# Kernel optimization log

Measured on AMD Instinct MI355X. Metric: run time of the kernel, lower is better.

## Reference

```python
import jax, jax.numpy as jnp
import numpy as np

B = 16384
IN = 1024      # feature_count * embedding_dim
E = 6          # expert_numb
D = 20         # domain_numb
EH1, EH2 = 256, 128
EO = 10        # expert_out_dim
GH = 64        # gate hidden
TH = 64        # tower hidden
TO = 1         # tower_output_dim


def setup_inputs() -> dict:
    key = jax.random.key(0)
    ks = jax.random.split(key, 20)
    s = lambda k, shp, fan: jax.random.normal(k, shp, jnp.float32) * (1.0 / np.sqrt(fan))
    return {
        "x": jax.random.normal(ks[0], (B, IN), jnp.float32),
        "domain_id": jax.random.randint(ks[1], (B,), 0, D, jnp.int64 if jax.config.jax_enable_x64 else jnp.int32),
        # expert MLPs: IN -> 256 -> 128 -> EO, ReLU hidden, no final act
        "Ew1": s(ks[2], (E, IN, EH1), IN), "Eb1": jnp.zeros((E, EH1), jnp.float32),
        "Ew2": s(ks[3], (E, EH1, EH2), EH1), "Eb2": jnp.zeros((E, EH2), jnp.float32),
        "Ew3": s(ks[4], (E, EH2, EO), EH2), "Eb3": jnp.zeros((E, EO), jnp.float32),
        # gate MLPs: IN -> 64 -> E, ReLU hidden, softmax applied in forward
        "Gw1": s(ks[5], (D, IN, GH), IN), "Gb1": jnp.zeros((D, GH), jnp.float32),
        "Gw2": s(ks[6], (D, GH, E), GH), "Gb2": jnp.zeros((D, E), jnp.float32),
        # tower MLPs: EO -> 64 -> 1, ReLU hidden, Sigmoid final
        "Tw1": s(ks[7], (D, EO, TH), EO), "Tb1": jnp.zeros((D, TH), jnp.float32),
        "Tw2": s(ks[8], (D, TH, TO), TH), "Tb2": jnp.zeros((D, TO), jnp.float32),
    }


def _forward(x, Ew1, Eb1, Ew2, Eb2, Ew3, Eb3, Gw1, Gb1, Gw2, Gb2, Tw1, Tb1, Tw2, Tb2, domain_id):
    # Experts: all E experts on every sample. eo: [E, B, EO]
    h = jax.nn.relu(jnp.einsum('bi,eih->ebh', x, Ew1) + Eb1[:, None, :])
    h = jax.nn.relu(jnp.einsum('ebh,ehk->ebk', h, Ew2) + Eb2[:, None, :])
    eo = jnp.einsum('ebk,eko->ebo', h, Ew3) + Eb3[:, None, :]
    # Gates: all D domain gates, softmax over expert axis. gate: [D, B, E]
    g = jax.nn.relu(jnp.einsum('bi,dih->dbh', x, Gw1) + Gb1[:, None, :])
    gate = jax.nn.softmax(jnp.einsum('dbh,dhe->dbe', g, Gw2) + Gb2[:, None, :], axis=-1)
    # MMoE combine per domain: [D, B, EO]
    mmoe = jnp.einsum('dbe,ebo->dbo', gate, eo)
    # Towers: all D towers. tout: [D, B, TO]
    th = jax.nn.relu(jnp.einsum('dbo,doh->dbh', mmoe, Tw1) + Tb1[:, None, :])
    tout = jax.nn.sigmoid(jnp.einsum('dbh,dho->dbo', th, Tw2) + Tb2[:, None, :])
    # Gather per-sample domain (discard 19/20 of tower & mmoe outputs)
    b_idx = jnp.arange(x.shape[0])
    selected_outputs = tout[domain_id, b_idx]   # [B, TO]
    selected_mmoe = mmoe[domain_id, b_idx]      # [B, EO]
    avg_expert_repr = jnp.mean(eo, axis=0)      # [B, EO]
    return selected_outputs, avg_expert_repr, selected_mmoe


def reference(x, domain_id, Ew1, Eb1, Ew2, Eb2, Ew3, Eb3, Gw1, Gb1, Gw2, Gb2, Tw1, Tb1, Tw2, Tb2):
    return _forward(x, Ew1, Eb1, Ew2, Eb2, Ew3, Eb3, Gw1, Gb1, Gw2, Gb2, Tw1, Tb1, Tw2, Tb2, domain_id)
```

## Files before the change

### kernel.cpp

```cpp
#include <hip/hip_runtime.h>
#include <hip/hip_bf16.h>
#include <math.h>

#define B_    16384
#define IN_   1024
#define E_    6
#define D_    20
#define EH1_  256
#define EH2_  128
#define EO_   10
#define GH_   64
#define TH_   64

typedef short  s16x8  __attribute__((ext_vector_type(8)));
typedef float  f32x4  __attribute__((ext_vector_type(4)));
typedef float  f32x16 __attribute__((ext_vector_type(16)));

__device__ inline ushort f2bf(float f) {
    union { float f; uint32_t u; } v; v.f = f;
    return (ushort)((v.u + 0x7fffu + ((v.u >> 16) & 1u)) >> 16);
}

#define GLOBAL_LDS16(g, l)                                                     \
    __builtin_amdgcn_global_load_lds(                                          \
        (const __attribute__((address_space(1))) void*)(g),                    \
        (__attribute__((address_space(3))) void*)(l), 16, 0, 0)

#define NCHUNK (B_ / 256)

#define CVT_BLKS  2048
#define CVT_ITERS (B_ * IN_ / 4 / 256 / CVT_BLKS)
#define WT1_TILES ((EH1_ / 32) * (IN_ / 32) * E_)
#define WT2_TILES ((EH2_ / 32) * (EH1_ / 32) * E_)
#define WTG_TILES ((GH_ / 32) * (IN_ / 32) * D_)
#define PREP_BLKS (CVT_BLKS + WT1_TILES + WT2_TILES + WTG_TILES + NCHUNK)

__global__ __launch_bounds__(256) void k_prep(
        const float* __restrict__ x, ushort* __restrict__ xb,
        const float* __restrict__ Ew1, ushort* __restrict__ W1t,
        const float* __restrict__ Ew2, ushort* __restrict__ W2t,
        const float* __restrict__ Gw1, ushort* __restrict__ G1t,
        const int* __restrict__ dom, int* __restrict__ cnts) {
    __shared__ float tile[32][33];
    __shared__ int hcnt[D_];
    int bid = blockIdx.x;
    const int t = threadIdx.x;

    if (bid < CVT_BLKS) {
        int i = bid * 256 + t;
        #pragma unroll
        for (int it = 0; it < CVT_ITERS; ++it, i += CVT_BLKS * 256) {
            float4 v = ((const float4*)x)[i];
            ushort4 o;
            o.x = f2bf(v.x); o.y = f2bf(v.y); o.z = f2bf(v.z); o.w = f2bf(v.w);
            ((ushort4*)xb)[i] = o;
        }
        return;
    }
    bid -= CVT_BLKS;

    const float* W; ushort* Wt; int K, N, z, ky, nx;
    if (bid < WT1_TILES) {
        W = Ew1; Wt = W1t; K = IN_; N = EH1_;
        z = bid / (8 * 32); int r = bid % (8 * 32); ky = r / 8; nx = r % 8;
    } else if (bid < WT1_TILES + WT2_TILES) {
        bid -= WT1_TILES;
        W = Ew2; Wt = W2t; K = EH1_; N = EH2_;
        z = bid / (4 * 8); int r = bid % (4 * 8); ky = r / 4; nx = r % 4;
    } else if (bid < WT1_TILES + WT2_TILES + WTG_TILES) {
        bid -= WT1_TILES + WT2_TILES;
        W = Gw1; Wt = G1t; K = IN_; N = GH_;
        z = bid / (2 * 32); int r = bid % (2 * 32); ky = r / 2; nx = r % 2;
    } else {
        int c = bid - (WT1_TILES + WT2_TILES + WTG_TILES);
        if (t < D_) hcnt[t] = 0;
        __syncthreads();
        atomicAdd(&hcnt[dom[c * 256 + t]], 1);
        __syncthreads();
        if (t < D_) cnts[c * D_ + t] = hcnt[t];
        return;
    }
    const int n0 = nx * 32, k0 = ky * 32;
    const float* We = W + (size_t)z * K * N;
    ushort* Wte = Wt + (size_t)z * K * N;
    const int lx = t & 31, ly = t >> 5;
    #pragma unroll
    for (int r = 0; r < 4; ++r)
        tile[ly + r * 8][lx] = We[(size_t)(k0 + ly + r * 8) * N + n0 + lx];
    __syncthreads();
    #pragma unroll
    for (int r = 0; r < 4; ++r)
        Wte[(size_t)(n0 + ly + r * 8) * K + k0 + lx] = f2bf(tile[lx][ly + r * 8]);
}

#define GBK 32
#define H2P 136

__global__ __launch_bounds__(256) void k_gemm(
        const ushort* __restrict__ A, const ushort* __restrict__ Wt,
        const float* __restrict__ Bias, ushort* __restrict__ C,
        const int* __restrict__ dom, const int* __restrict__ cnts,
        int* __restrict__ perm, int* __restrict__ gbaseG,
        int* __restrict__ histG, int* __restrict__ gtab,
        int* __restrict__ ngt) {
    __shared__ __attribute__((aligned(16))) ushort As[128 * GBK];
    __shared__ __attribute__((aligned(16))) ushort Bs[128 * GBK];

    const int t = threadIdx.x;

    if (blockIdx.z == 0 && blockIdx.x == 0 && blockIdx.y < NCHUNK) {
        int* cl    = (int*)As;
        int* tot   = cl + NCHUNK * D_;
        int* lbase = tot + D_;
        int* lcnt  = lbase + D_;
        const int c = blockIdx.y;

        for (int i = t; i < NCHUNK * D_; i += 256) cl[i] = cnts[i];
        __syncthreads();
        if (t < D_) {
            int before = 0, total = 0;
            #pragma unroll 8
            for (int cc = 0; cc < NCHUNK; ++cc) {
                int v = cl[cc * D_ + t];
                if (cc < c) before += v;
                total += v;
            }
            tot[t] = total; lbase[t] = before; lcnt[t] = 0;
        }
        __syncthreads();
        if (t < D_) {
            int gb = 0;
            #pragma unroll
            for (int d2 = 0; d2 < D_; ++d2) if (d2 < t) gb += tot[d2];
            lbase[t] += gb;
            if (c == 0) { gbaseG[t] = gb; histG[t] = tot[t]; }
        }
        __syncthreads();
        if (c == 0 && t < D_) {
            int off = 0, nt = (tot[t] + 63) >> 6;
            #pragma unroll
            for (int d2 = 0; d2 < D_; ++d2)
                if (d2 < t) off += (tot[d2] + 63) >> 6;
            for (int tt = 0; tt < nt; ++tt) gtab[off + tt] = (t << 16) | tt;
            if (t == D_ - 1) ngt[0] = off + nt;
        }
        {
            const int g = c * 256 + t;
            const int d = dom[g];
            int r = atomicAdd(&lcnt[d], 1);
            perm[lbase[d] + r] = g;
        }
        __syncthreads();
    }

    const int e = blockIdx.z;
    const ushort* Ae = A;
    const ushort* We = Wt + (size_t)e * (size_t)EH1_ * IN_;
    const float* BiasE = Bias + (size_t)e * EH1_;
    ushort* Ce = C + (size_t)e * (size_t)B_ * EH1_;

    const int m0 = blockIdx.y * 128;
    const int n0 = blockIdx.x * 128;
    const int wave = t >> 6;
    const int lane = t & 63;

    const int q0 = wave * 2, q1 = q0 + 1;
    const int sr0 = q0 * 16 + (lane >> 2);
    const int sr1 = sr0 + 16;
    const int sw  = ((lane & 3) ^ ((sr0 >> 1) & 3)) * 8;

    const int l32  = lane & 31;
    const int ksel = lane >> 5;
    const int rw = (wave & 1) * 64;
    const int cw = (wave >> 1) * 64;

    int rowA[2], rowB[2], swzA[2], swzB[2];
    #pragma unroll
    for (int i = 0; i < 2; ++i) {
        rowA[i] = rw + 32 * i + l32;  swzA[i] = (rowA[i] >> 1) & 3;
        rowB[i] = cw + 32 * i + l32;  swzB[i] = (rowB[i] >> 1) & 3;
    }

    f32x16 acc[2][2] = {};

    for (int k0 = 0; k0 < IN_; k0 += GBK) {
        GLOBAL_LDS16(Ae + (size_t)(m0 + sr0) * IN_ + k0 + sw, As + q0 * 512);
        GLOBAL_LDS16(Ae + (size_t)(m0 + sr1) * IN_ + k0 + sw, As + q1 * 512);
        GLOBAL_LDS16(We + (size_t)(n0 + sr0) * IN_ + k0 + sw, Bs + q0 * 512);
        GLOBAL_LDS16(We + (size_t)(n0 + sr1) * IN_ + k0 + sw, Bs + q1 * 512);
        __syncthreads();

        #pragma unroll
        for (int h = 0; h < 2; ++h) {
            const int cb = h * 2 + ksel;
            s16x8 af[2], bf[2];
            #pragma unroll
            for (int i = 0; i < 2; ++i)
                af[i] = *(const s16x8*)&As[rowA[i] * GBK + ((cb ^ swzA[i]) * 8)];
            #pragma unroll
            for (int j = 0; j < 2; ++j)
                bf[j] = *(const s16x8*)&Bs[rowB[j] * GBK + ((cb ^ swzB[j]) * 8)];
            #pragma unroll
            for (int i = 0; i < 2; ++i)
                #pragma unroll
                for (int j = 0; j < 2; ++j)
                    acc[i][j] = __builtin_amdgcn_mfma_f32_32x32x16_bf16(
                        af[i], bf[j], acc[i][j], 0, 0, 0);
        }
        __syncthreads();
    }

    float bi[2];
    #pragma unroll
    for (int j = 0; j < 2; ++j) bi[j] = BiasE[n0 + cw + 32 * j + l32];

    #pragma unroll
    for (int i = 0; i < 2; ++i) {
        #pragma unroll
        for (int reg = 0; reg < 16; ++reg) {
            int rowin = (reg & 3) + 8 * (reg >> 2) + 4 * ksel;
            ushort* crow = Ce + (size_t)(m0 + rw + 32 * i + rowin) * EH1_;
            #pragma unroll
            for (int j = 0; j < 2; ++j) {
                float v = fmaxf(acc[i][j][reg] + bi[j], 0.f);
                crow[n0 + cw + 32 * j + l32] = f2bf(v);
            }
        }
    }
}

#define GYL (E_ + 3)

__global__ __launch_bounds__(256) void k_l2eog(
        const ushort* __restrict__ h1, const ushort* __restrict__ W2t,
        const float* __restrict__ Eb2, const float* __restrict__ Ew3,
        const float* __restrict__ Eb3, float* __restrict__ eo,
        const ushort* __restrict__ xb, const ushort* __restrict__ Gw1t,
        const float* __restrict__ Gb1, const float* __restrict__ Gw2,
        const float* __restrict__ Gb2, const int* __restrict__ perm,
        const int* __restrict__ histG, const int* __restrict__ gbaseG,
        const int* __restrict__ gtab, const int* __restrict__ ngt,
        float* __restrict__ gate) {
    __shared__ __attribute__((aligned(16))) ushort smem[17408 + 16 * H2P];

    const int t = threadIdx.x;
    const int wave = t >> 6;
    const int lane = t & 63;
    const int quad = lane >> 4;
    const int l16  = lane & 15;
    const int l32  = lane & 31;
    const int ksel = lane >> 5;

    if (blockIdx.y < E_) {
        ushort* As = smem;
        ushort* Bs = smem + 4096;

        const int e = blockIdx.y;
        const ushort* Ae = h1 + (size_t)e * B_ * EH1_;
        const ushort* We = W2t + (size_t)e * EH2_ * EH1_;

        const int m0 = blockIdx.x * 128;

        const int q0 = wave * 2, q1 = q0 + 1;
        const int sr0 = q0 * 16 + (lane >> 2);
        const int sr1 = sr0 + 16;
        const int sw  = ((lane & 3) ^ ((sr0 >> 1) & 3)) * 8;

        const int rw = (wave & 1) * 64;
        const int cw = (wave >> 1) * 64;

        int rowA[2], rowB[2], swzA[2], swzB[2];
        #pragma unroll
        for (int i = 0; i < 2; ++i) {
            rowA[i] = rw + 32 * i + l32;  swzA[i] = (rowA[i] >> 1) & 3;
            rowB[i] = cw + 32 * i + l32;  swzB[i] = (rowB[i] >> 1) & 3;
        }

        f32x16 acc[2][2] = {};

        for (int k0 = 0; k0 < EH1_; k0 += GBK) {
            GLOBAL_LDS16(Ae + (size_t)(m0 + sr0) * EH1_ + k0 + sw, As + q0 * 512);
            GLOBAL_LDS16(Ae + (size_t)(m0 + sr1) * EH1_ + k0 + sw, As + q1 * 512);
            GLOBAL_LDS16(We + (size_t)sr0 * EH1_ + k0 + sw, Bs + q0 * 512);
            GLOBAL_LDS16(We + (size_t)sr1 * EH1_ + k0 + sw, Bs + q1 * 512);
            __syncthreads();

            #pragma unroll
            for (int h = 0; h < 2; ++h) {
                const int cb = h * 2 + ksel;
                s16x8 af[2], bf[2];
                #pragma unroll
                for (int i = 0; i < 2; ++i)
                    af[i] = *(const s16x8*)&As[rowA[i] * GBK + ((cb ^ swzA[i]) * 8)];
                #pragma unroll
                for (int j = 0; j < 2; ++j)
                    bf[j] = *(const s16x8*)&Bs[rowB[j] * GBK + ((cb ^ swzB[j]) * 8)];
                #pragma unroll
                for (int i = 0; i < 2; ++i)
                    #pragma unroll
                    for (int j = 0; j < 2; ++j)
                        acc[i][j] = __builtin_amdgcn_mfma_f32_32x32x16_bf16(
                            af[i], bf[j], acc[i][j], 0, 0, 0);
            }
            __syncthreads();
        }

        ushort* h2L = smem;
        ushort* E3t = smem + 128 * H2P;

        float bi[2];
        #pragma unroll
        for (int j = 0; j < 2; ++j) bi[j] = Eb2[e * EH2_ + cw + 32 * j + l32];

        #pragma unroll
        for (int i = 0; i < 2; ++i)
            #pragma unroll
            for (int reg = 0; reg < 16; ++reg) {
                int rowin = (reg & 3) + 8 * (reg >> 2) + 4 * ksel;
                int row = rw + 32 * i + rowin;
                #pragma unroll
                for (int j = 0; j < 2; ++j)
                    h2L[row * H2P + cw + 32 * j + l32] =
                        f2bf(fmaxf(acc[i][j][reg] + bi[j], 0.f));
            }

        for (int i = t; i < 16 * 128; i += 256) {
            int col = i >> 7, k = i & 127;
            float v = (col < EO_) ? Ew3[(size_t)e * EH2_ * EO_ + k * EO_ + col] : 0.f;
            E3t[col * H2P + k] = f2bf(v);
        }
        __syncthreads();

        #pragma unroll
        for (int gi = 0; gi < 2; ++gi) {
            int g = wave * 2 + gi;
            f32x4 acc2 = {};
            #pragma unroll
            for (int kc = 0; kc < 4; ++kc) {
                s16x8 a = *(const s16x8*)&h2L[(g * 16 + l16) * H2P + kc * 32 + quad * 8];
                s16x8 b = *(const s16x8*)&E3t[l16 * H2P + kc * 32 + quad * 8];
                acc2 = __builtin_amdgcn_mfma_f32_16x16x32_bf16(a, b, acc2, 0, 0, 0);
            }
            if (l16 < EO_) {
                float b3 = Eb3[e * EO_ + l16];
                #pragma unroll
                for (int r = 0; r < 4; ++r) {
                    int row = m0 + g * 16 + quad * 4 + r;
                    eo[(size_t)row * (E_ * EO_) + e * EO_ + l16] = acc2[r] + b3;
                }
            }
        }
        return;
    }

    {
        const int gidx = (blockIdx.y - E_) * gridDim.x + blockIdx.x;
        if (gidx >= ngt[0]) return;
        const int entry = gtab[gidx];
        const int d     = entry >> 16;
        const int start = (entry & 0xffff) * 64;
        const int base  = gbaseG[d];
        const int cnt   = histG[d];

        ushort* gAs  = smem;
        ushort* gBs  = smem + 2048;
        int*    ridx = (int*)(smem + 4096);
        float (*gh)[GH_ + 1] = (float(*)[GH_ + 1])(smem + 4224);
        float*  w2s  = (float*)(smem + 12544);
        float*  b2s  = (float*)(smem + 13312);
        float (*lg)[E_] = (float(*)[E_])(smem + 13324);

        const int qsw = (quad ^ ((l16 >> 1) & 3)) * 8;

        if (t < 64) {
            int p = start + t;
            ridx[t] = (p < cnt) ? perm[base + p] : perm[base];
        }
        for (int i = t; i < GH_ * E_; i += 256) w2s[i] = Gw2[(size_t)d * GH_ * E_ + i];
        if (t < E_) b2s[t] = Gb2[d * E_ + t];
        __syncthreads();

        const int srow = t >> 2;
        const int sw   = ((t & 3) ^ ((srow >> 1) & 3)) * 8;
        const int myRow = ridx[srow];
        const ushort* aRow = xb + (size_t)myRow * IN_ + sw;
        const ushort* bRow = Gw1t + (size_t)d * GH_ * IN_ + (size_t)srow * IN_ + sw;

        f32x4 acc[4] = {};
        for (int k0 = 0; k0 < IN_; k0 += 32) {
            GLOBAL_LDS16(aRow + k0, gAs + wave * 512);
            GLOBAL_LDS16(bRow + k0, gBs + wave * 512);
            __syncthreads();

            s16x8 bf = *(const s16x8*)&gBs[(wave * 16 + l16) * 32 + qsw];
            #pragma unroll
            for (int i = 0; i < 4; ++i) {
                s16x8 af = *(const s16x8*)&gAs[(16 * i + l16) * 32 + qsw];
                acc[i] = __builtin_amdgcn_mfma_f32_16x16x32_bf16(af, bf, acc[i], 0, 0, 0);
            }
            __syncthreads();
        }

        const int hcol = wave * 16 + l16;
        float hb = Gb1[d * GH_ + hcol];
        #pragma unroll
        for (int i = 0; i < 4; ++i)
            #pragma unroll
            for (int r = 0; r < 4; ++r)
                gh[16 * i + quad * 4 + r][hcol] = fmaxf(acc[i][r] + hb, 0.f);
        __syncthreads();

        for (int p = t; p < 64 * E_; p += 256) {
            int row = p / E_, e = p - row * E_;
            float s = b2s[e];
            #pragma unroll 8
            for (int h = 0; h < GH_; ++h) s += gh[row][h] * w2s[h * E_ + e];
            lg[row][e] = s;
        }
        __syncthreads();

        if (t < 64 && start + t < cnt) {
            int b = ridx[t];
            float mx = lg[t][0];
            #pragma unroll
            for (int e = 1; e < E_; ++e) mx = fmaxf(mx, lg[t][e]);
            float ex[E_], sum = 0.f;
            #pragma unroll
            for (int e = 0; e < E_; ++e) { ex[e] = expf(lg[t][e] - mx); sum += ex[e]; }
            float inv = 1.f / sum;
            #pragma unroll
            for (int e = 0; e < E_; ++e) gate[(size_t)b * E_ + e] = ex[e] * inv;
        }
    }
}

__global__ __launch_bounds__(256) void k_final(
        const float* __restrict__ eo, const float* __restrict__ gate,
        const int* __restrict__ dom,
        const float* __restrict__ Tw1, const float* __restrict__ Tb1,
        const float* __restrict__ Tw2, const float* __restrict__ Tb2,
        float* __restrict__ out) {
    const int wave = threadIdx.x >> 6;
    const int lane = threadIdx.x & 63;
    const int b = blockIdx.x * 4 + wave;
    const int d = dom[b];

    const float* eob = eo + (size_t)b * (E_ * EO_);
    float g[E_];
    #pragma unroll
    for (int e = 0; e < E_; ++e) g[e] = gate[(size_t)b * E_ + e];

    float mmoe[EO_], avg[EO_];
    #pragma unroll
    for (int o = 0; o < EO_; ++o) {
        float m = 0.f, a = 0.f;
        #pragma unroll
        for (int e = 0; e < E_; ++e) {
            float v = eob[e * EO_ + o];
            m += g[e] * v;
            a += v;
        }
        mmoe[o] = m;
        avg[o] = a * (1.0f / E_);
    }

    float acc = Tb1[d * TH_ + lane];
    #pragma unroll
    for (int o = 0; o < EO_; ++o)
        acc += mmoe[o] * Tw1[(size_t)d * EO_ * TH_ + o * TH_ + lane];
    acc = fmaxf(acc, 0.f);

    float s = acc * Tw2[d * TH_ + lane];
    #pragma unroll
    for (int off = 32; off >= 1; off >>= 1) s += __shfl_xor(s, off, 64);

    if (lane == 0)
        out[b] = 1.f / (1.f + expf(-(s + Tb2[d])));
    if (lane < EO_) {
        out[B_ + (size_t)b * EO_ + lane] = avg[lane];
        out[B_ + (size_t)B_ * EO_ + (size_t)b * EO_ + lane] = mmoe[lane];
    }
}

extern "C" void kernel_launch(void* const* d_in, const int* in_sizes, int n_in,
                              void* d_out, int out_size, void* d_ws, size_t ws_size,
                              hipStream_t stream) {
    const float* x   = (const float*)d_in[0];
    const int*   dom = (const int*)d_in[1];
    const float* Ew1 = (const float*)d_in[2];
    const float* Eb1 = (const float*)d_in[3];
    const float* Ew2 = (const float*)d_in[4];
    const float* Eb2 = (const float*)d_in[5];
    const float* Ew3 = (const float*)d_in[6];
    const float* Eb3 = (const float*)d_in[7];
    const float* Gw1 = (const float*)d_in[8];
    const float* Gb1 = (const float*)d_in[9];
    const float* Gw2 = (const float*)d_in[10];
    const float* Gb2 = (const float*)d_in[11];
    const float* Tw1 = (const float*)d_in[12];
    const float* Tb1 = (const float*)d_in[13];
    const float* Tw2 = (const float*)d_in[14];
    const float* Tb2 = (const float*)d_in[15];
    float* out = (float*)d_out;

    char* ws = (char*)d_ws;
    size_t off = 0;
    auto take = [&](size_t bytes) -> char* {
        char* p = ws + off;
        off = (off + bytes + 255) & ~(size_t)255;
        return p;
    };
    int*    cnts    = (int*)take((size_t)NCHUNK * D_ * 4);
    int*    histG   = (int*)take(D_ * 4);
    int*    gbaseG  = (int*)take(D_ * 4);
    int*    gtab    = (int*)take(512 * 4);
    int*    ngt     = (int*)take(4);
    int*    perm    = (int*)take(B_ * 4);
    float*  gateBuf = (float*)take((size_t)B_ * E_ * 4);
    float*  eoBuf   = (float*)take((size_t)B_ * E_ * EO_ * 4);
    ushort* xb      = (ushort*)take((size_t)B_ * IN_ * 2);
    ushort* W1t     = (ushort*)take((size_t)E_ * IN_ * EH1_ * 2);
    ushort* W2t     = (ushort*)take((size_t)E_ * EH1_ * EH2_ * 2);
    ushort* G1t     = (ushort*)take((size_t)D_ * IN_ * GH_ * 2);
    ushort* h1      = (ushort*)take((size_t)E_ * B_ * EH1_ * 2);

    k_prep<<<dim3(PREP_BLKS), dim3(256), 0, stream>>>(
        x, xb, Ew1, W1t, Ew2, W2t, Gw1, G1t, dom, cnts);

    k_gemm<<<dim3(EH1_ / 128, B_ / 128, E_), dim3(256), 0, stream>>>(
        xb, W1t, Eb1, h1, dom, cnts, perm, gbaseG, histG, gtab, ngt);

    k_l2eog<<<dim3(B_ / 128, GYL), dim3(256), 0, stream>>>(
        h1, W2t, Eb2, Ew3, Eb3, eoBuf,
        xb, G1t, Gb1, Gw2, Gb2, perm, histG, gbaseG, gtab, ngt, gateBuf);

    k_final<<<dim3(B_ / 4), dim3(256), 0, stream>>>(
        eoBuf, gateBuf, dom, Tw1, Tb1, Tw2, Tb2, out);
}
```

Before: 241.1 us.

## Use 64x64 transpose tiles in prep and remap GEMM block order for locality

The weight transpose/convert in the prep kernel now uses 64x64 LDS tiles with 16 rows per thread, giving fewer, larger blocks. The first GEMM kernel remaps its linear block index so that consecutive blocks, interleaved across 8 groups, cover nearby M tiles and both N tiles of one expert. The remap aims at better L2 reuse of A and weight tiles, and possibly a better spread across XCDs. Larger tiles raise LDS use and per-thread work in prep and may lower occupancy.

Result: no change. 240.3 us (-0.3%).

```diff
diff --git a/kernel.cpp b/kernel.cpp
--- a/kernel.cpp
+++ b/kernel.cpp
@@ -30,10 +30,10 @@
 
 #define CVT_BLKS  2048
 #define CVT_ITERS (B_ * IN_ / 4 / 256 / CVT_BLKS)
-#define WT1_TILES ((EH1_ / 32) * (IN_ / 32) * E_)
-#define WT2_TILES ((EH2_ / 32) * (EH1_ / 32) * E_)
-#define WTG_TILES ((GH_ / 32) * (IN_ / 32) * D_)
-#define PREP_BLKS (CVT_BLKS + WT1_TILES + WT2_TILES + WTG_TILES + NCHUNK)
+#define WT1_T64 (E_ * (EH1_ / 64) * (IN_ / 64))
+#define WT2_T64 (E_ * (EH2_ / 64) * (EH1_ / 64))
+#define WTG_T64 (D_ * (GH_ / 64) * (IN_ / 64))
+#define PREP_BLKS (CVT_BLKS + WT1_T64 + WT2_T64 + WTG_T64 + NCHUNK)
 
 __global__ __launch_bounds__(256) void k_prep(
         const float* __restrict__ x, ushort* __restrict__ xb,
@@ -41,7 +41,7 @@
         const float* __restrict__ Ew2, ushort* __restrict__ W2t,
         const float* __restrict__ Gw1, ushort* __restrict__ G1t,
         const int* __restrict__ dom, int* __restrict__ cnts) {
-    __shared__ float tile[32][33];
+    __shared__ float tile[64][65];
     __shared__ int hcnt[D_];
     int bid = blockIdx.x;
     const int t = threadIdx.x;
@@ -60,19 +60,19 @@
     bid -= CVT_BLKS;
 
     const float* W; ushort* Wt; int K, N, z, ky, nx;
-    if (bid < WT1_TILES) {
+    if (bid < WT1_T64) {
         W = Ew1; Wt = W1t; K = IN_; N = EH1_;
-        z = bid / (8 * 32); int r = bid % (8 * 32); ky = r / 8; nx = r % 8;
-    } else if (bid < WT1_TILES + WT2_TILES) {
-        bid -= WT1_TILES;
+        z = bid / (4 * 16); int r = bid % (4 * 16); ky = r / 4; nx = r % 4;
+    } else if (bid < WT1_T64 + WT2_T64) {
+        bid -= WT1_T64;
         W = Ew2; Wt = W2t; K = EH1_; N = EH2_;
-        z = bid / (4 * 8); int r = bid % (4 * 8); ky = r / 4; nx = r % 4;
-    } else if (bid < WT1_TILES + WT2_TILES + WTG_TILES) {
-        bid -= WT1_TILES + WT2_TILES;
+        z = bid / (2 * 4); int r = bid % (2 * 4); ky = r / 2; nx = r % 2;
+    } else if (bid < WT1_T64 + WT2_T64 + WTG_T64) {
+        bid -= WT1_T64 + WT2_T64;
         W = Gw1; Wt = G1t; K = IN_; N = GH_;
-        z = bid / (2 * 32); int r = bid % (2 * 32); ky = r / 2; nx = r % 2;
+        z = bid / 16; ky = bid % 16; nx = 0;
     } else {
-        int c = bid - (WT1_TILES + WT2_TILES + WTG_TILES);
+        int c = bid - (WT1_T64 + WT2_T64 + WTG_T64);
         if (t < D_) hcnt[t] = 0;
         __syncthreads();
         atomicAdd(&hcnt[dom[c * 256 + t]], 1);
@@ -80,17 +80,18 @@
         if (t < D_) cnts[c * D_ + t] = hcnt[t];
         return;
     }
-    const int n0 = nx * 32, k0 = ky * 32;
+    const int n0 = nx * 64, k0 = ky * 64;
     const float* We = W + (size_t)z * K * N;
     ushort* Wte = Wt + (size_t)z * K * N;
-    const int lx = t & 31, ly = t >> 5;
-    #pragma unroll
-    for (int r = 0; r < 4; ++r)
-        tile[ly + r * 8][lx] = We[(size_t)(k0 + ly + r * 8) * N + n0 + lx];
+    const int lx = t & 63, ly = t >> 6;
+    #pragma unroll
+    for (int r = 0; r < 16; ++r)
+        tile[ly * 16 + r][lx] = We[(size_t)(k0 + ly * 16 + r) * N + n0 + lx];
     __syncthreads();
     #pragma unroll
-    for (int r = 0; r < 4; ++r)
-        Wte[(size_t)(n0 + ly + r * 8) * K + k0 + lx] = f2bf(tile[lx][ly + r * 8]);
+    for (int r = 0; r < 16; ++r)
+        Wte[(size_t)(n0 + ly * 16 + r) * K + k0 + lx] =
+            f2bf(tile[lx][ly * 16 + r]);
 }
 
 #define GBK 32
@@ -108,12 +109,19 @@
 
     const int t = threadIdx.x;
 
-    if (blockIdx.z == 0 && blockIdx.x == 0 && blockIdx.y < NCHUNK) {
+    const int lin = blockIdx.x + 2 * blockIdx.y + 256 * blockIdx.z;
+    const int q  = lin & 7;
+    const int rr = lin >> 3;
+    const int by = q * 16 + (rr & 15);
+    const int bx = (rr >> 4) & 1;
+    const int bz = rr >> 5;
+
+    if (bz == 0 && bx == 0 && by < NCHUNK) {
         int* cl    = (int*)As;
         int* tot   = cl + NCHUNK * D_;
         int* lbase = tot + D_;
         int* lcnt  = lbase + D_;
-        const int c = blockIdx.y;
+        const int c = by;
 
         for (int i = t; i < NCHUNK * D_; i += 256) cl[i] = cnts[i];
         __syncthreads();
@@ -153,14 +161,14 @@
         __syncthreads();
     }
 
-    const int e = blockIdx.z;
+    const int e = bz;
     const ushort* Ae = A;
     const ushort* We = Wt + (size_t)e * (size_t)EH1_ * IN_;
     const float* BiasE = Bias + (size_t)e * EH1_;
     ushort* Ce = C + (size_t)e * (size_t)B_ * EH1_;
 
-    const int m0 = blockIdx.y * 128;
-    const int n0 = blockIdx.x * 128;
+    const int m0 = by * 128;
+    const int n0 = bx * 128;
     const int wave = t >> 6;
     const int lane = t & 63;
 
```
